# Kernel tuning notes

Measured on AMD Instinct MI355X. Metric: run time of the kernel, lower is better.

Reference implementation:

```python
import jax, jax.numpy as jnp
import numpy as np

EPS = 1e-5  # torch GroupNorm default


def setup_inputs() -> dict:
    key = jax.random.key(0)
    ks = jax.random.split(key, 7)
    B, H, W, C = 8, 64, 64, 64
    x = jax.random.normal(ks[0], (B, H, W, C), dtype=jnp.float32)
    temb = jax.random.normal(ks[1], (B, 256), dtype=jnp.float32)
    scale = 0.02
    Wq = jax.random.normal(ks[2], (C, C), dtype=jnp.float32) * scale
    Wk = jax.random.normal(ks[3], (C, C), dtype=jnp.float32) * scale
    Wv = jax.random.normal(ks[4], (C, C), dtype=jnp.float32) * scale
    Wo = jax.random.normal(ks[5], (C, C), dtype=jnp.float32) * scale
    z = jnp.zeros((C,), dtype=jnp.float32)
    return {"x": x, "temb": temb, "Wq": Wq, "bq": z, "Wk": Wk, "bk": z,
            "Wv": Wv, "bv": z, "Wo": Wo, "bo": z}


def reference(x, temb, Wq, bq, Wk, bk, Wv, bv, Wo, bo):
    # x: [B, H, W, C] channels-last. temb is accepted but unused (as in source).
    B, H, W, C = x.shape
    S = H * W
    # normalize(): freshly-built GroupNorm(num_groups=1) with identity affine
    # -> standardize over all non-batch dims.
    mu = jnp.mean(x, axis=(1, 2, 3), keepdims=True)
    var = jnp.var(x, axis=(1, 2, 3), keepdims=True)
    h = (x - mu) * jax.lax.rsqrt(var + EPS)
    hf = h.reshape(B, S, C)
    q = hf @ Wq.T + bq  # [B, S, C]
    k = hf @ Wk.T + bk
    v = hf @ Wv.T + bv
    # full (S x S) score matrix, scaled by C^-0.5, naive softmax
    w = jnp.einsum('bsc,btc->bst', q, k) * (C ** -0.5)
    w = jax.nn.softmax(w, axis=-1)
    o = jnp.einsum('bst,btc->bsc', w, v)  # [B, S, C]
    o = o @ Wo.T + bo
    return x + o.reshape(B, H, W, C)
```

## Files before the change

kernel.cpp:

```cpp
#include <hip/hip_runtime.h>
#include <hip/hip_bf16.h>
#include <math.h>

#define B_ 8
#define S_ 4096
#define C_ 64
#define EPSV 1e-5f

using floatx4 = __attribute__((ext_vector_type(4))) float;
using bf16x8  = __attribute__((ext_vector_type(8))) short;
using bf16x4  = __attribute__((ext_vector_type(4))) short;

typedef __attribute__((address_space(3))) unsigned int       as3_u32;
typedef __attribute__((address_space(1))) const unsigned int as1_u32;

__device__ __forceinline__ short f2bf(float f) {
    unsigned u = __builtin_bit_cast(unsigned, f);
    u = u + 0x7fffu + ((u >> 16) & 1u);
    return (short)(u >> 16);
}

__device__ __forceinline__ float bf2f(short s) {
    return __builtin_bit_cast(float, ((unsigned)(unsigned short)s) << 16);
}

__device__ __forceinline__ unsigned cvt_pk_bf16(float lo, float hi) {
    unsigned r;
    asm volatile("v_cvt_pk_bf16_f32 %0, %1, %2" : "=v"(r) : "v"(lo), "v"(hi));
    return r;
}

__device__ __forceinline__ floatx4 mfma_16x16x16_bf16(bf16x4 a, bf16x4 b, floatx4 c) {
#if __has_builtin(__builtin_amdgcn_mfma_f32_16x16x16bf16_1k)
    return __builtin_amdgcn_mfma_f32_16x16x16bf16_1k(a, b, c, 0, 0, 0);
#else
    asm("v_mfma_f32_16x16x16_bf16 %0, %1, %2, %0" : "+v"(c) : "v"(a), "v"(b));
    return c;
#endif
}

__device__ __forceinline__ bf16x8 ld_w_frag(const float* __restrict__ W, int n, int kk, int g, int c) {
    const float* p = W + (16 * n + c) * C_ + 32 * kk + 8 * g;
    bf16x8 r;
#pragma unroll
    for (int j = 0; j < 8; ++j) r[j] = f2bf(p[j]);
    return r;
}

__global__ __launch_bounds__(256) void stats1_kernel(const float* __restrict__ x,
                                                     float* __restrict__ partial) {
    int b = blockIdx.x >> 5, chunk = blockIdx.x & 31;
    const float4* xb = (const float4*)x + (size_t)b * 65536 + chunk * 2048;
    float s = 0.f, ss = 0.f;
#pragma unroll
    for (int i = 0; i < 8; ++i) {
        float4 v = xb[threadIdx.x + i * 256];
        s  += v.x + v.y + v.z + v.w;
        ss += v.x * v.x + v.y * v.y + v.z * v.z + v.w * v.w;
    }
    for (int off = 32; off > 0; off >>= 1) {
        s  += __shfl_down(s, off);
        ss += __shfl_down(ss, off);
    }
    __shared__ float sm[4], ssm[4];
    int wid = threadIdx.x >> 6, lane = threadIdx.x & 63;
    if (lane == 0) { sm[wid] = s; ssm[wid] = ss; }
    __syncthreads();
    if (threadIdx.x == 0) {
        partial[blockIdx.x * 2]     = sm[0] + sm[1] + sm[2] + sm[3];
        partial[blockIdx.x * 2 + 1] = ssm[0] + ssm[1] + ssm[2] + ssm[3];
    }
}

__global__ __launch_bounds__(512) void stats2_kernel(const float* __restrict__ partial,
                                                     float* __restrict__ stats) {
    int w = threadIdx.x >> 6, lane = threadIdx.x & 63;
    float s = 0.f, ss = 0.f;
    if (lane < 32) {
        s  = partial[(w * 32 + lane) * 2];
        ss = partial[(w * 32 + lane) * 2 + 1];
    }
    for (int off = 16; off > 0; off >>= 1) {
        s  += __shfl_down(s, off);
        ss += __shfl_down(ss, off);
    }
    if (lane == 0) {
        const float invN = 1.0f / (float)(S_ * C_);
        float mu  = s * invN;
        float var = ss * invN - mu * mu;
        stats[w * 2]     = mu;
        stats[w * 2 + 1] = rsqrtf(var + EPSV);
    }
}

__global__ __launch_bounds__(256) void proj_kernel(
    const float* __restrict__ x,
    const float* __restrict__ Wq, const float* __restrict__ bq,
    const float* __restrict__ Wk, const float* __restrict__ bk,
    const float* __restrict__ Wv, const float* __restrict__ bv,
    const float* __restrict__ stats,
    short* __restrict__ qo, char* __restrict__ kws, char* __restrict__ vws) {
    __shared__ char hbuf[8192];
    __shared__ char kimg[8192];
    __shared__ char vimg[8192];

    int b  = blockIdx.x >> 6;
    int t_ = blockIdx.x & 63;
    int s0 = t_ * 64;
    float mu = stats[b * 2], rs = stats[b * 2 + 1];
    const float* xt = x + ((size_t)b * S_ + s0) * C_;
    int t = threadIdx.x;

#pragma unroll
    for (int i = 0; i < 4; ++i) {
        int fi  = t + 256 * i;
        int row = fi >> 4;
        int c4  = fi & 15;
        float4 v = *(const float4*)(xt + row * C_ + c4 * 4);
        unsigned lo = (unsigned)(unsigned short)f2bf((v.x - mu) * rs) |
                      ((unsigned)(unsigned short)f2bf((v.y - mu) * rs) << 16);
        unsigned hi = (unsigned)(unsigned short)f2bf((v.z - mu) * rs) |
                      ((unsigned)(unsigned short)f2bf((v.w - mu) * rs) << 16);
        int off = row * 128 + c4 * 8;
        off ^= (row & 7) << 4;
        *(uint2*)(hbuf + off) = make_uint2(lo, hi);
    }
    __syncthreads();

    int lane = t & 63, w = t >> 6;
    int g = lane >> 4, c = lane & 15;

    auto ld_h = [&](int row, int kcol) -> bf16x8 {
        int off = row * 128 + kcol * 2;
        off ^= (row & 7) << 4;
        return *(const bf16x8*)(hbuf + off);
    };

    bf16x8 ha[2];
    ha[0] = ld_h(16 * w + c, 8 * g);
    ha[1] = ld_h(16 * w + c, 32 + 8 * g);

    const float QSC = 0.125f * 1.44269504088896340736f;

#pragma unroll
    for (int n = 0; n < 4; ++n) {
        floatx4 aq = {0.f, 0.f, 0.f, 0.f}, ak = {0.f, 0.f, 0.f, 0.f};
#pragma unroll
        for (int kk = 0; kk < 2; ++kk) {
            bf16x8 wq = ld_w_frag(Wq, n, kk, g, c);
            bf16x8 wk = ld_w_frag(Wk, n, kk, g, c);
            aq = __builtin_amdgcn_mfma_f32_16x16x32_bf16(ha[kk], wq, aq, 0, 0, 0);
            ak = __builtin_amdgcn_mfma_f32_16x16x32_bf16(ha[kk], wk, ak, 0, 0, 0);
        }
        float bqv = bq[16 * n + c], bkv = bk[16 * n + c];
#pragma unroll
        for (int r = 0; r < 4; ++r) {
            int rr = 16 * w + 4 * g + r;
            qo[((size_t)b * S_ + s0 + rr) * C_ + 16 * n + c] = f2bf((aq[r] + bqv) * QSC);
            int r32 = rr & 31;
            int koff = (r32 * 128 + (16 * n + c) * 2) ^ ((r32 & 7) << 4);
            *(short*)(kimg + (rr >> 5) * 4096 + koff) = f2bf(ak[r] + bkv);
        }
    }

    bf16x8 wv[2];
    wv[0] = ld_w_frag(Wv, w, 0, g, c);
    wv[1] = ld_w_frag(Wv, w, 1, g, c);
    float bvr[4];
#pragma unroll
    for (int r = 0; r < 4; ++r) bvr[r] = bv[16 * w + 4 * g + r];

#pragma unroll
    for (int n = 0; n < 4; ++n) {
        floatx4 av = {0.f, 0.f, 0.f, 0.f};
#pragma unroll
        for (int kk = 0; kk < 2; ++kk) {
            bf16x8 hb = ld_h(16 * n + c, 32 * kk + 8 * g);
            av = __builtin_amdgcn_mfma_f32_16x16x32_bf16(wv[kk], hb, av, 0, 0, 0);
        }
        int u   = 16 * n + c;
        int u32 = u & 31;
#pragma unroll
        for (int r = 0; r < 4; ++r) {
            int rr = 16 * w + 4 * g + r;
            int voff = (rr * 64 + u32 * 2) ^ ((rr & 7) << 3);
            *(short*)(vimg + (u >> 5) * 4096 + voff) = f2bf(av[r] + bvr[r]);
        }
    }
    __syncthreads();

    size_t gb = ((size_t)b * 128 + 2 * t_) * 4096;
#pragma unroll
    for (int i = 0; i < 2; ++i) {
        *(uint4*)(kws + gb + i * 4096 + t * 16) = *(const uint4*)(kimg + i * 4096 + t * 16);
        *(uint4*)(vws + gb + i * 4096 + t * 16) = *(const uint4*)(vimg + i * 4096 + t * 16);
    }
}

__global__ __launch_bounds__(256, 4) void flash_kernel(
    const short* __restrict__ qm, const char* __restrict__ kws, const char* __restrict__ vws,
    short* __restrict__ Opart, float2* __restrict__ mlpart) {
    __shared__ char lds[24576];

    int bid = blockIdx.x;
    int logical = (bid & 7) * 128 + (bid >> 3);
    int b = logical >> 7;
    int rest = logical & 127;
    int q0 = (rest >> 2) * 128;
    int quarter = rest & 3;
    int t = threadIdx.x;
    int lane = t & 63, w = t >> 6;
    int g = lane >> 4, c = lane & 15;
    int qw = q0 + 32 * w;

    const char* kbase = kws + (size_t)b * 128 * 4096;
    const char* vbase = vws + (size_t)b * 128 * 4096;
    const short* qp = qm + (size_t)b * S_ * C_;

    bf16x8 bqf[2][2];
#pragma unroll
    for (int qi = 0; qi < 2; ++qi) {
        bqf[qi][0] = *(const bf16x8*)(qp + (qw + 16 * qi + c) * C_ + 8 * g);
        bqf[qi][1] = *(const bf16x8*)(qp + (qw + 16 * qi + c) * C_ + 32 + 8 * g);
    }

    floatx4 oacc[2][4];
#pragma unroll
    for (int qi = 0; qi < 2; ++qi)
#pragma unroll
        for (int mi = 0; mi < 4; ++mi) oacc[qi][mi] = (floatx4){0.f, 0.f, 0.f, 0.f};
    float m[2] = {-__builtin_inff(), -__builtin_inff()}, l[2] = {0.f, 0.f};

    const int xmask  = (c & 7) << 4;
    const int vxmask = (c & 7) << 3;

    auto STAGE = [&](int bi, int tt) {
        const char* gk = kbase + (size_t)tt * 4096 + t * 16;
        const char* gv = vbase + (size_t)tt * 4096 + t * 16;
        char* lk = lds +         bi * 4096 + t * 16;
        char* lv = lds + 12288 + bi * 4096 + t * 16;
        __builtin_amdgcn_global_load_lds((as1_u32*)gk, (as3_u32*)lk, 16, 0, 0);
        __builtin_amdgcn_global_load_lds((as1_u32*)gv, (as3_u32*)lv, 16, 0, 0);
    };

    auto ld_k = [&](const char* buf, int s, int colb) -> bf16x8 {
        return *(const bf16x8*)(buf + s * 2048 + c * 128 + (colb ^ xmask));
    };
    auto ld_v = [&](const char* buf, int mi, int s) -> bf16x4 {
        return *(const bf16x4*)(buf + mi * 1024 + c * 64 + ((32 * s + 8 * g) ^ vxmask));
    };

    auto COMPUTE = [&](int bi) {
        const char* kbuf = lds +         bi * 4096;
        const char* vbuf = lds + 12288 + bi * 4096;
        bf16x8 ak[2][2];
#pragma unroll
        for (int s = 0; s < 2; ++s)
#pragma unroll
            for (int kk = 0; kk < 2; ++kk)
                ak[s][kk] = ld_k(kbuf, s, 64 * kk + 16 * g);
        floatx4 st[2][2];
        __builtin_amdgcn_s_setprio(1);
#pragma unroll
        for (int qi = 0; qi < 2; ++qi)
#pragma unroll
            for (int s = 0; s < 2; ++s) {
                st[qi][s] = (floatx4){0.f, 0.f, 0.f, 0.f};
                st[qi][s] = __builtin_amdgcn_mfma_f32_16x16x32_bf16(ak[s][0], bqf[qi][0], st[qi][s], 0, 0, 0);
                st[qi][s] = __builtin_amdgcn_mfma_f32_16x16x32_bf16(ak[s][1], bqf[qi][1], st[qi][s], 0, 0, 0);
            }
        __builtin_amdgcn_s_setprio(0);
        bf16x4 av[2][4];
#pragma unroll
        for (int s = 0; s < 2; ++s)
#pragma unroll
            for (int mi = 0; mi < 4; ++mi)
                av[s][mi] = ld_v(vbuf, mi, s);
        float mt[2], need = -1e30f;
#pragma unroll
        for (int qi = 0; qi < 2; ++qi) {
            float v = fmaxf(fmaxf(st[qi][0][0], st[qi][0][1]), fmaxf(st[qi][0][2], st[qi][0][3]));
            v = fmaxf(v, fmaxf(fmaxf(st[qi][1][0], st[qi][1][1]), fmaxf(st[qi][1][2], st[qi][1][3])));
            v = fmaxf(v, __shfl_xor(v, 16));
            v = fmaxf(v, __shfl_xor(v, 32));
            mt[qi] = v;
            need = fmaxf(need, v - m[qi]);
        }
        if (!__all(need <= 8.0f)) {
#pragma unroll
            for (int qi = 0; qi < 2; ++qi) {
                float mn = fmaxf(m[qi], mt[qi]);
                float a  = __builtin_amdgcn_exp2f(m[qi] - mn);
                m[qi] = mn;
                l[qi] *= a;
#pragma unroll
                for (int mi = 0; mi < 4; ++mi) oacc[qi][mi] *= a;
            }
        }
        bf16x4 pb[2][2];
#pragma unroll
        for (int qi = 0; qi < 2; ++qi) {
            float psum = 0.f;
#pragma unroll
            for (int s = 0; s < 2; ++s) {
                float e0 = __builtin_amdgcn_exp2f(st[qi][s][0] - m[qi]);
                float e1 = __builtin_amdgcn_exp2f(st[qi][s][1] - m[qi]);
                float e2 = __builtin_amdgcn_exp2f(st[qi][s][2] - m[qi]);
                float e3 = __builtin_amdgcn_exp2f(st[qi][s][3] - m[qi]);
                psum += (e0 + e1) + (e2 + e3);
                uint2 u = make_uint2(cvt_pk_bf16(e0, e1), cvt_pk_bf16(e2, e3));
                pb[qi][s] = __builtin_bit_cast(bf16x4, u);
            }
            l[qi] += psum;
        }
        __builtin_amdgcn_s_setprio(1);
#pragma unroll
        for (int qi = 0; qi < 2; ++qi)
#pragma unroll
            for (int s = 0; s < 2; ++s)
#pragma unroll
                for (int mi = 0; mi < 4; ++mi)
                    oacc[qi][mi] = mfma_16x16x16_bf16(av[s][mi], pb[qi][s], oacc[qi][mi]);
        __builtin_amdgcn_s_setprio(0);
    };

    const int base = quarter * 32;
    STAGE(0, base);
    STAGE(1, base + 1);
    asm volatile("s_waitcnt vmcnt(2)" ::: "memory");
    __builtin_amdgcn_s_barrier();
    __builtin_amdgcn_sched_barrier(0);

    for (int r = 0; r < 32; ++r) {
        if (r < 30) STAGE((r + 2) % 3, base + r + 2);
        COMPUTE(r % 3);
        if (r < 31) {
            if (r < 30) asm volatile("s_waitcnt vmcnt(2)" ::: "memory");
            else        asm volatile("s_waitcnt vmcnt(0)" ::: "memory");
            __builtin_amdgcn_s_barrier();
            __builtin_amdgcn_sched_barrier(0);
        }
    }

#pragma unroll
    for (int qi = 0; qi < 2; ++qi) {
        l[qi] += __shfl_xor(l[qi], 16);
        l[qi] += __shfl_xor(l[qi], 32);
    }

    size_t prow = (size_t)(quarter * 8 + b) * S_ + q0;
    if (lane < 16) {
#pragma unroll
        for (int qi = 0; qi < 2; ++qi)
            mlpart[prow + 32 * w + 16 * qi + lane] = make_float2(m[qi], l[qi]);
    }

#pragma unroll
    for (int qi = 0; qi < 2; ++qi) {
        short* op = Opart + (prow + 32 * w + 16 * qi + c) * C_;
#pragma unroll
        for (int mi = 0; mi < 4; ++mi) {
            uint2 u = make_uint2(cvt_pk_bf16(oacc[qi][mi][0], oacc[qi][mi][1]),
                                 cvt_pk_bf16(oacc[qi][mi][2], oacc[qi][mi][3]));
            *(uint2*)(op + 16 * mi + 4 * g) = u;
        }
    }
}

__global__ __launch_bounds__(256) void combine_kernel(
    const short* __restrict__ Opart, const float2* __restrict__ mlpart,
    const float* __restrict__ Wo, const float* __restrict__ bo,
    const float* __restrict__ x, float* __restrict__ out) {
    __shared__ char obuf[8192];

    int bid = blockIdx.x;
    int logical = (bid & 7) * 64 + (bid >> 3);
    int b = logical >> 6;
    int q0 = (logical & 63) * 64;
    int t = threadIdx.x;
    int lane = t & 63, w = t >> 6;
    int g = lane >> 4, c = lane & 15;

    const short*  P[4];
    const float2* ml[4];
#pragma unroll
    for (int h = 0; h < 4; ++h) {
        P[h]  = Opart  + ((size_t)(h * 8 + b) * S_ + q0) * C_;
        ml[h] = mlpart + (size_t)(h * 8 + b) * S_ + q0;
    }

#pragma unroll
    for (int i = 0; i < 16; ++i) {
        int idx = t + 256 * i;
        int q = idx >> 6, ch = idx & 63;
        float2 a0 = ml[0][q], a1 = ml[1][q], a2 = ml[2][q], a3 = ml[3][q];
        float M = fmaxf(fmaxf(a0.x, a1.x), fmaxf(a2.x, a3.x));
        float s0 = __builtin_amdgcn_exp2f(a0.x - M);
        float s1 = __builtin_amdgcn_exp2f(a1.x - M);
        float s2 = __builtin_amdgcn_exp2f(a2.x - M);
        float s3 = __builtin_amdgcn_exp2f(a3.x - M);
        float L  = a0.y * s0 + a1.y * s1 + a2.y * s2 + a3.y * s3;
        float o  = (bf2f(P[0][q * 64 + ch]) * s0 + bf2f(P[1][q * 64 + ch]) * s1 +
                    bf2f(P[2][q * 64 + ch]) * s2 + bf2f(P[3][q * 64 + ch]) * s3) / L;
        int off = (q * 128 + ch * 2) ^ ((q & 7) << 4);
        *(short*)(obuf + off) = f2bf(o);
    }
    __syncthreads();

    bf16x8 ao[2];
    {
        int row = 16 * w + c;
        int off0 = (row * 128 + (8 * g) * 2)      ^ ((row & 7) << 4);
        int off1 = (row * 128 + (32 + 8 * g) * 2) ^ ((row & 7) << 4);
        ao[0] = *(const bf16x8*)(obuf + off0);
        ao[1] = *(const bf16x8*)(obuf + off1);
    }
#pragma unroll
    for (int n = 0; n < 4; ++n) {
        floatx4 a = {0.f, 0.f, 0.f, 0.f};
#pragma unroll
        for (int kk = 0; kk < 2; ++kk) {
            bf16x8 bw = ld_w_frag(Wo, n, kk, g, c);
            a = __builtin_amdgcn_mfma_f32_16x16x32_bf16(ao[kk], bw, a, 0, 0, 0);
        }
        float bov = bo[16 * n + c];
#pragma unroll
        for (int r = 0; r < 4; ++r) {
            int srow = q0 + 16 * w + 4 * g + r;
            size_t idx = ((size_t)b * S_ + srow) * C_ + 16 * n + c;
            out[idx] = x[idx] + bov + a[r];
        }
    }
}

extern "C" void kernel_launch(void* const* d_in, const int* in_sizes, int n_in,
                              void* d_out, int out_size, void* d_ws, size_t ws_size,
                              hipStream_t stream) {
    const float* x  = (const float*)d_in[0];
    const float* Wq = (const float*)d_in[2];
    const float* bq = (const float*)d_in[3];
    const float* Wk = (const float*)d_in[4];
    const float* bk = (const float*)d_in[5];
    const float* Wv = (const float*)d_in[6];
    const float* bv = (const float*)d_in[7];
    const float* Wo = (const float*)d_in[8];
    const float* bo = (const float*)d_in[9];
    float* out = (float*)d_out;

    char* ws = (char*)d_ws;
    float*  partial = (float*)ws;
    float*  stats   = (float*)(ws + 2048);
    short*  q   = (short*)(ws + 4096);
    char*   kt  = (char*)(q + (size_t)B_ * S_ * C_);
    char*   vt  = kt + (size_t)B_ * 128 * 4096;
    short*  op  = (short*)(vt + (size_t)B_ * 128 * 4096);
    float2* mlp = (float2*)((char*)op + (size_t)4 * B_ * S_ * C_ * 2);

    stats1_kernel<<<256, 256, 0, stream>>>(x, partial);
    stats2_kernel<<<1, 512, 0, stream>>>(partial, stats);
    proj_kernel<<<B_ * (S_ / 64), 256, 0, stream>>>(x, Wq, bq, Wk, bk, Wv, bv, stats, q, kt, vt);
    flash_kernel<<<B_ * (S_ / 128) * 4, 256, 0, stream>>>(q, kt, vt, op, mlp);
    combine_kernel<<<B_ * (S_ / 64), 256, 0, stream>>>(op, mlp, Wo, bo, x, out);
}
```

Measured before the change: 88.63 us.

## Use 16x16x32 MFMA for PV product via ds_bpermute P-fragment reshuffle

Measured after the change: 91.72 us. 3.5% more time.

```diff
diff --git a/kernel.cpp b/kernel.cpp
--- a/kernel.cpp
+++ b/kernel.cpp
@@ -10,6 +10,7 @@
 using floatx4 = __attribute__((ext_vector_type(4))) float;
 using bf16x8  = __attribute__((ext_vector_type(8))) short;
 using bf16x4  = __attribute__((ext_vector_type(4))) short;
+using intx4   = __attribute__((ext_vector_type(4))) int;
 
 typedef __attribute__((address_space(3))) unsigned int       as3_u32;
 typedef __attribute__((address_space(1))) const unsigned int as1_u32;
@@ -28,15 +29,6 @@
     unsigned r;
     asm volatile("v_cvt_pk_bf16_f32 %0, %1, %2" : "=v"(r) : "v"(lo), "v"(hi));
     return r;
-}
-
-__device__ __forceinline__ floatx4 mfma_16x16x16_bf16(bf16x4 a, bf16x4 b, floatx4 c) {
-#if __has_builtin(__builtin_amdgcn_mfma_f32_16x16x16bf16_1k)
-    return __builtin_amdgcn_mfma_f32_16x16x16bf16_1k(a, b, c, 0, 0, 0);
-#else
-    asm("v_mfma_f32_16x16x16_bf16 %0, %1, %2, %0" : "+v"(c) : "v"(a), "v"(b));
-    return c;
-#endif
 }
 
 __device__ __forceinline__ bf16x8 ld_w_frag(const float* __restrict__ W, int n, int kk, int g, int c) {
@@ -183,7 +175,7 @@
 #pragma unroll
         for (int r = 0; r < 4; ++r) {
             int rr = 16 * w + 4 * g + r;
-            int voff = (rr * 64 + u32 * 2) ^ ((rr & 7) << 3);
+            int voff = (rr * 64 + u32 * 2) ^ (((rr >> 1) & 3) << 4);
             *(short*)(vimg + (u >> 5) * 4096 + voff) = f2bf(av[r] + bvr[r]);
         }
     }
@@ -232,7 +224,10 @@
     float m[2] = {-__builtin_inff(), -__builtin_inff()}, l[2] = {0.f, 0.f};
 
     const int xmask  = (c & 7) << 4;
-    const int vxmask = (c & 7) << 3;
+    const int vxmask = ((c >> 1) & 3) << 4;
+    const int addr0 = (32 * (g & 1) + c) * 4;
+    const int addr1 = addr0 + 64;
+    const bool kbhi = (g >> 1) != 0;
 
     auto STAGE = [&](int bi, int tt) {
         const char* gk = kbase + (size_t)tt * 4096 + t * 16;
@@ -246,8 +241,8 @@
     auto ld_k = [&](const char* buf, int s, int colb) -> bf16x8 {
         return *(const bf16x8*)(buf + s * 2048 + c * 128 + (colb ^ xmask));
     };
-    auto ld_v = [&](const char* buf, int mi, int s) -> bf16x4 {
-        return *(const bf16x4*)(buf + mi * 1024 + c * 64 + ((32 * s + 8 * g) ^ vxmask));
+    auto ld_v = [&](const char* buf, int mi) -> bf16x8 {
+        return *(const bf16x8*)(buf + mi * 1024 + c * 64 + ((16 * g) ^ vxmask));
     };
 
     auto COMPUTE = [&](int bi) {
@@ -270,12 +265,10 @@
                 st[qi][s] = __builtin_amdgcn_mfma_f32_16x16x32_bf16(ak[s][1], bqf[qi][1], st[qi][s], 0, 0, 0);
             }
         __builtin_amdgcn_s_setprio(0);
-        bf16x4 av[2][4];
-#pragma unroll
-        for (int s = 0; s < 2; ++s)
-#pragma unroll
-            for (int mi = 0; mi < 4; ++mi)
-                av[s][mi] = ld_v(vbuf, mi, s);
+        bf16x8 av[4];
+#pragma unroll
+        for (int mi = 0; mi < 4; ++mi)
+            av[mi] = ld_v(vbuf, mi);
         float mt[2], need = -1e30f;
 #pragma unroll
         for (int qi = 0; qi < 2; ++qi) {
@@ -297,30 +290,40 @@
                 for (int mi = 0; mi < 4; ++mi) oacc[qi][mi] *= a;
             }
         }
-        bf16x4 pb[2][2];
+        __builtin_amdgcn_s_setprio(1);
 #pragma unroll
         for (int qi = 0; qi < 2; ++qi) {
-            float psum = 0.f;
-#pragma unroll
-            for (int s = 0; s < 2; ++s) {
-                float e0 = __builtin_amdgcn_exp2f(st[qi][s][0] - m[qi]);
-                float e1 = __builtin_amdgcn_exp2f(st[qi][s][1] - m[qi]);
-                float e2 = __builtin_amdgcn_exp2f(st[qi][s][2] - m[qi]);
-                float e3 = __builtin_amdgcn_exp2f(st[qi][s][3] - m[qi]);
-                psum += (e0 + e1) + (e2 + e3);
-                uint2 u = make_uint2(cvt_pk_bf16(e0, e1), cvt_pk_bf16(e2, e3));
-                pb[qi][s] = __builtin_bit_cast(bf16x4, u);
-            }
-            l[qi] += psum;
-        }
-        __builtin_amdgcn_s_setprio(1);
-#pragma unroll
-        for (int qi = 0; qi < 2; ++qi)
-#pragma unroll
-            for (int s = 0; s < 2; ++s)
-#pragma unroll
-                for (int mi = 0; mi < 4; ++mi)
-                    oacc[qi][mi] = mfma_16x16x16_bf16(av[s][mi], pb[qi][s], oacc[qi][mi]);
+            float e0 = __builtin_amdgcn_exp2f(st[qi][0][0] - m[qi]);
+            float e1 = __builtin_amdgcn_exp2f(st[qi][0][1] - m[qi]);
+            float e2 = __builtin_amdgcn_exp2f(st[qi][0][2] - m[qi]);
+            float e3 = __builtin_amdgcn_exp2f(st[qi][0][3] - m[qi]);
+            float e4 = __builtin_amdgcn_exp2f(st[qi][1][0] - m[qi]);
+            float e5 = __builtin_amdgcn_exp2f(st[qi][1][1] - m[qi]);
+            float e6 = __builtin_amdgcn_exp2f(st[qi][1][2] - m[qi]);
+            float e7 = __builtin_amdgcn_exp2f(st[qi][1][3] - m[qi]);
+            l[qi] += ((e0 + e1) + (e2 + e3)) + ((e4 + e5) + (e6 + e7));
+            unsigned pk00 = cvt_pk_bf16(e0, e1);
+            unsigned pk01 = cvt_pk_bf16(e2, e3);
+            unsigned pk10 = cvt_pk_bf16(e4, e5);
+            unsigned pk11 = cvt_pk_bf16(e6, e7);
+            int w0a = __builtin_amdgcn_ds_bpermute(addr0, (int)pk00);
+            int w0b = __builtin_amdgcn_ds_bpermute(addr0, (int)pk10);
+            int w1a = __builtin_amdgcn_ds_bpermute(addr0, (int)pk01);
+            int w1b = __builtin_amdgcn_ds_bpermute(addr0, (int)pk11);
+            int w2a = __builtin_amdgcn_ds_bpermute(addr1, (int)pk00);
+            int w2b = __builtin_amdgcn_ds_bpermute(addr1, (int)pk10);
+            int w3a = __builtin_amdgcn_ds_bpermute(addr1, (int)pk01);
+            int w3b = __builtin_amdgcn_ds_bpermute(addr1, (int)pk11);
+            intx4 bpw;
+            bpw[0] = kbhi ? w0b : w0a;
+            bpw[1] = kbhi ? w1b : w1a;
+            bpw[2] = kbhi ? w2b : w2a;
+            bpw[3] = kbhi ? w3b : w3a;
+            bf16x8 bp = __builtin_bit_cast(bf16x8, bpw);
+#pragma unroll
+            for (int mi = 0; mi < 4; ++mi)
+                oacc[qi][mi] = __builtin_amdgcn_mfma_f32_16x16x32_bf16(av[mi], bp, oacc[qi][mi], 0, 0, 0);
+        }
         __builtin_amdgcn_s_setprio(0);
     };
 
```
